# Optimization experiments

Measured on AMD Instinct MI355X. Metric: run time of the kernel, lower is better.

Reference implementation:

```python
import jax, jax.numpy as jnp
import numpy as np

NEG = -1e30

def setup_inputs() -> dict:
    key = jax.random.key(0)
    k = jax.random.split(key, 6)
    B, Lc, Lq, D = 16, 2048, 256, 256
    c = jax.random.normal(k[0], (B, Lc, D), dtype=jnp.float32)
    q = jax.random.normal(k[1], (B, Lq, D), dtype=jnp.float32)
    c_mask = jnp.ones((B, Lc), dtype=jnp.float32)
    q_mask = jnp.ones((B, Lq), dtype=jnp.float32)
    # xavier-uniform-ish scale for the similarity weights
    lim = float(np.sqrt(6.0 / (D + 1)))
    cq_weight = jax.random.uniform(k[2], (1, 1, D), jnp.float32, -lim, lim)
    c_weight = jax.random.uniform(k[3], (1, D), jnp.float32, -lim, lim)
    q_weight = jax.random.uniform(k[4], (1, D), jnp.float32, -lim, lim)
    bias = jnp.zeros((1,), dtype=jnp.float32)
    return {"c": c, "q": q, "c_mask": c_mask, "q_mask": q_mask,
            "cq_weight": cq_weight, "c_weight": c_weight,
            "q_weight": q_weight, "bias": bias}

def _masked_softmax(logits, mask):
    # mask: 1=keep, 0=pad; broadcast over logits' leading dims
    x = logits * mask + (1.0 - mask) * NEG
    return jax.nn.softmax(x, axis=-1)

def reference(c, q, c_mask, q_mask, cq_weight, c_weight, q_weight, bias):
    # trilinear similarity S[b,i,j] = w_c.c_i + w_q.q_j + (c_i*w_cq).q_j + b
    s0 = jnp.einsum('bid,od->bio', c, c_weight)              # [B,Lc,1]
    s1 = jnp.einsum('bjd,od->boj', q, q_weight)              # [B,1,Lq]
    s2 = jnp.einsum('bid,bjd->bij', c * cq_weight, q)        # [B,Lc,Lq]
    S = s0 + s1 + s2 + bias                                  # [B,Lc,Lq]
    S1 = _masked_softmax(S, q_mask[:, None, :])              # softmax over q
    C2Q = jnp.einsum('bij,bjd->bid', S1, q)                  # [B,Lc,D]
    S2t = _masked_softmax(jnp.swapaxes(S, 1, 2), c_mask[:, None, :])  # [B,Lq,Lc]
    S2 = jnp.einsum('bij,bjk->bik', S1, S2t)                 # [B,Lc,Lc]
    Q2C = jnp.einsum('bik,bkd->bid', S2, c)                  # [B,Lc,D]
    return jnp.concatenate((c, C2Q, c * C2Q, c * Q2C), axis=-1)
```

## Files before the change

kernel.cpp:

```cpp
#include <hip/hip_runtime.h>
#include <hip/hip_bf16.h>

#define NB 16
#define LC 2048
#define LQ 256
#define DD 256
#define NEGINF -1e30f

typedef __attribute__((ext_vector_type(8))) short bf16x8;
typedef __attribute__((ext_vector_type(4))) float f32x4;

#define MFMA16(a, b, c) __builtin_amdgcn_mfma_f32_16x16x32_bf16((a), (b), (c), 0, 0, 0)

typedef const unsigned int __attribute__((address_space(1))) glb_u32;
typedef unsigned int __attribute__((address_space(3))) lds_u32;

__device__ __forceinline__ void gload_lds16(const void* g, void* l) {
    __builtin_amdgcn_global_load_lds((glb_u32*)g, (lds_u32*)l, 16, 0, 0);
}

__device__ __forceinline__ short f2b(float x) {
    unsigned u = __float_as_uint(x);
    unsigned r = (u + 0x7fffu + ((u >> 16) & 1u)) >> 16;
    return (short)r;
}
__device__ __forceinline__ float b2f(short s) {
    return __uint_as_float(((unsigned)(unsigned short)s) << 16);
}

#define NCB (NB * LC / 8)
__global__ __launch_bounds__(256) void prep(
        const float* __restrict__ c, const float* __restrict__ q,
        const float* __restrict__ c_w, const float* __restrict__ cqw,
        const float* __restrict__ q_w, const float* __restrict__ bias,
        short* __restrict__ c16, float* __restrict__ s0c,
        short* __restrict__ qw16, short* __restrict__ qT16,
        float* __restrict__ s1q) {
    __shared__ float T[64][65];
    int t = threadIdx.x;
    if (blockIdx.x < NCB) {
        int row = blockIdx.x * 8 + (t >> 5);
        int k = t & 31;
        const float* src = c + (size_t)row * DD + k * 8;
        float4 v0 = *(const float4*)(src);
        float4 v1 = *(const float4*)(src + 4);
        float4 w0 = *(const float4*)(c_w + k * 8);
        float4 w1 = *(const float4*)(c_w + k * 8 + 4);
        float s = v0.x * w0.x + v0.y * w0.y + v0.z * w0.z + v0.w * w0.w
                + v1.x * w1.x + v1.y * w1.y + v1.z * w1.z + v1.w * w1.w;
        #pragma unroll
        for (int o = 16; o > 0; o >>= 1) s += __shfl_xor(s, o, 64);
        if (k == 0) s0c[row] = s;
        ushort4 o0, o1;
        o0.x = (unsigned short)f2b(v0.x); o0.y = (unsigned short)f2b(v0.y);
        o0.z = (unsigned short)f2b(v0.z); o0.w = (unsigned short)f2b(v0.w);
        o1.x = (unsigned short)f2b(v1.x); o1.y = (unsigned short)f2b(v1.y);
        o1.z = (unsigned short)f2b(v1.z); o1.w = (unsigned short)f2b(v1.w);
        ushort4* dst = (ushort4*)(c16 + (size_t)row * DD + k * 8);
        dst[0] = o0;
        dst[1] = o1;
    } else {
        int idx = blockIdx.x - NCB;
        int b = idx >> 2, j0 = (idx & 3) * 64;
        int dd = t & 63, rg = t >> 6;
        float acc[16];
        #pragma unroll
        for (int i = 0; i < 16; ++i) acc[i] = 0.f;
        for (int dc = 0; dc < 4; ++dc) {
            float wv = cqw[dc * 64 + dd];
            float qwv = q_w[dc * 64 + dd];
            #pragma unroll
            for (int rr = 0; rr < 16; ++rr) {
                int r = rg + 4 * rr;
                float v = q[((size_t)b * LQ + j0 + r) * DD + dc * 64 + dd];
                qw16[((size_t)b * LQ + j0 + r) * DD + dc * 64 + dd] = f2b(v * wv);
                acc[rr] += v * qwv;
                T[dd][r] = v;
            }
            __syncthreads();
            int jj = t & 63;
            for (int dw = t >> 6; dw < 64; dw += 4)
                qT16[((size_t)b * DD + dc * 64 + dw) * LQ + j0 + jj] = f2b(T[dw][jj]);
            __syncthreads();
        }
        float bv = bias[0];
        #pragma unroll
        for (int rr = 0; rr < 16; ++rr) {
            float s = acc[rr];
            #pragma unroll
            for (int o = 32; o > 0; o >>= 1) s += __shfl_xor(s, o, 64);
            if (dd == 0) s1q[b * LQ + j0 + rg + 4 * rr] = s + bv;
        }
    }
}

__global__ __launch_bounds__(512) void k1_S(
        const short* __restrict__ c16, const short* __restrict__ qw16,
        const float* __restrict__ cmask, const float* __restrict__ qmask,
        const float* __restrict__ s0c, const float* __restrict__ s1q,
        short* __restrict__ P1b, float* __restrict__ wgtg,
        float* __restrict__ pm, float* __restrict__ ps) {
    __shared__ short As[128 * 64];
    __shared__ short Bs[256 * 64];
    __shared__ float rmLds[128 * 4];
    __shared__ float rsLds[128 * 4];
    __shared__ float rowCLds[128];
    int b  = blockIdx.y;
    int i0 = blockIdx.x * 128;
    int t = threadIdx.x;
    int l = t & 63, w = t >> 6;
    int wr = w >> 2, wc = w & 3;

    f32x4 acc[4][4];
    #pragma unroll
    for (int m = 0; m < 4; ++m)
        #pragma unroll
        for (int n = 0; n < 4; ++n) acc[m][n] = (f32x4){0.f, 0.f, 0.f, 0.f};

    const short* Ag = c16  + ((size_t)b * LC + i0) * DD;
    const short* Bg = qw16 + ((size_t)b * LQ) * DD;
    int lrow = l >> 3;
    int lcolsw = ((l & 7) ^ lrow) * 8;

    for (int kt = 0; kt < DD; kt += 64) {
        __syncthreads();
        #pragma unroll
        for (int r = 0; r < 2; ++r) {
            int chunk = r * 8 + w;
            int row = chunk * 8 + lrow;
            gload_lds16(Ag + (size_t)row * DD + kt + lcolsw, As + chunk * 512);
        }
        #pragma unroll
        for (int r = 0; r < 4; ++r) {
            int chunk = r * 8 + w;
            int row = chunk * 8 + lrow;
            gload_lds16(Bg + (size_t)row * DD + kt + lcolsw, Bs + chunk * 512);
        }
        __syncthreads();
        #pragma unroll
        for (int kf = 0; kf < 2; ++kf) {
            bf16x8 a[4], bb[4];
            #pragma unroll
            for (int m = 0; m < 4; ++m) {
                int row = wr * 64 + m * 16 + (l & 15);
                int byte = row * 128 + kf * 64 + (l >> 4) * 16;
                a[m] = *(const bf16x8*)((const char*)As + (byte ^ ((row & 7) << 4)));
            }
            #pragma unroll
            for (int n = 0; n < 4; ++n) {
                int row = wc * 64 + n * 16 + (l & 15);
                int byte = row * 128 + kf * 64 + (l >> 4) * 16;
                bb[n] = *(const bf16x8*)((const char*)Bs + (byte ^ ((row & 7) << 4)));
            }
            #pragma unroll
            for (int m = 0; m < 4; ++m)
                #pragma unroll
                for (int n = 0; n < 4; ++n)
                    acc[m][n] = MFMA16(a[m], bb[n], acc[m][n]);
        }
    }

    float s1v[4], qmv[4], negq[4];
    #pragma unroll
    for (int n = 0; n < 4; ++n) {
        int j = wc * 64 + n * 16 + (l & 15);
        s1v[n] = s1q[b * LQ + j];
        qmv[n] = qmask[b * LQ + j];
        negq[n] = (1.f - qmv[n]) * NEGINF;
    }
    float s0r[4][4], cmr[4][4];
    #pragma unroll
    for (int m = 0; m < 4; ++m)
        #pragma unroll
        for (int reg = 0; reg < 4; ++reg) {
            int il = wr * 64 + m * 16 + (l >> 4) * 4 + reg;
            s0r[m][reg] = s0c[b * LC + i0 + il];
            cmr[m][reg] = cmask[b * LC + i0 + il];
        }
    #pragma unroll
    for (int m = 0; m < 4; ++m)
        #pragma unroll
        for (int n = 0; n < 4; ++n)
            #pragma unroll
            for (int reg = 0; reg < 4; ++reg)
                acc[m][n][reg] = acc[m][n][reg] + s0r[m][reg] + s1v[n];

    #pragma unroll
    for (int n = 0; n < 4; ++n) {
        float x2v[16];
        float mx = NEGINF;
        #pragma unroll
        for (int m = 0; m < 4; ++m)
            #pragma unroll
            for (int reg = 0; reg < 4; ++reg) {
                float cm = cmr[m][reg];
                float x2 = acc[m][n][reg] * cm + (1.f - cm) * NEGINF;
                x2v[m * 4 + reg] = x2;
                mx = fmaxf(mx, x2);
            }
        float ss = 0.f;
        #pragma unroll
        for (int e = 0; e < 16; ++e) ss += __expf(x2v[e] - mx);
        #pragma unroll
        for (int off = 16; off <= 32; off <<= 1) {
            float om = __shfl_xor(mx, off, 64);
            float os = __shfl_xor(ss, off, 64);
            float nm = fmaxf(mx, om);
            ss = ss * __expf(mx - nm) + os * __expf(om - nm);
            mx = nm;
        }
        if (l < 16) {
            size_t idx = ((size_t)b * 32 + blockIdx.x * 2 + wr) * LQ + wc * 64 + n * 16 + l;
            pm[idx] = mx;
            ps[idx] = ss;
        }
    }

    #pragma unroll
    for (int m = 0; m < 4; ++m)
        #pragma unroll
        for (int reg = 0; reg < 4; ++reg) {
            float mx = NEGINF;
            #pragma unroll
            for (int n = 0; n < 4; ++n)
                mx = fmaxf(mx, fmaf(acc[m][n][reg], qmv[n], negq[n]));
            #pragma unroll
            for (int o = 1; o <= 8; o <<= 1) mx = fmaxf(mx, __shfl_xor(mx, o, 64));
            float ss = 0.f;
            #pragma unroll
            for (int n = 0; n < 4; ++n)
                ss += __expf(fmaf(acc[m][n][reg], qmv[n], negq[n]) - mx);
            #pragma unroll
            for (int o = 1; o <= 8; o <<= 1) ss += __shfl_xor(ss, o, 64);
            if ((l & 15) == 0) {
                int row = wr * 64 + m * 16 + (l >> 4) * 4 + reg;
                rmLds[row * 4 + wc] = mx;
                rsLds[row * 4 + wc] = ss;
            }
        }
    __syncthreads();
    if (t < 128) {
        float m0 = rmLds[t * 4 + 0], m1 = rmLds[t * 4 + 1];
        float m2 = rmLds[t * 4 + 2], m3 = rmLds[t * 4 + 3];
        float mm = fmaxf(fmaxf(m0, m1), fmaxf(m2, m3));
        float ss = rsLds[t * 4 + 0] * __expf(m0 - mm)
                 + rsLds[t * 4 + 1] * __expf(m1 - mm)
                 + rsLds[t * 4 + 2] * __expf(m2 - mm)
                 + rsLds[t * 4 + 3] * __expf(m3 - mm);
        float rc = mm + logf(ss);
        rowCLds[t] = rc;
        wgtg[(size_t)b * LC + i0 + t] = cmask[b * LC + i0 + t] * __expf(rc);
    }
    __syncthreads();

    float rCv[4][4];
    #pragma unroll
    for (int m = 0; m < 4; ++m)
        #pragma unroll
        for (int reg = 0; reg < 4; ++reg)
            rCv[m][reg] = rowCLds[wr * 64 + m * 16 + (l >> 4) * 4 + reg];
    #pragma unroll
    for (int m = 0; m < 4; ++m)
        #pragma unroll
        for (int n = 0; n < 4; ++n)
            #pragma unroll
            for (int reg = 0; reg < 4; ++reg) {
                float p = __expf(fmaf(acc[m][n][reg], qmv[n], negq[n]) - rCv[m][reg]);
                int il = wr * 64 + m * 16 + (l >> 4) * 4 + reg;
                int j = wc * 64 + n * 16 + (l & 15);
                P1b[((size_t)b * LC + i0 + il) * LQ + j] = f2b(p);
            }
}

#define K3S 72
__global__ __launch_bounds__(256) void k3_A2C(
        const short* __restrict__ c16, const short* __restrict__ P1b,
        const float* __restrict__ wgtg,
        float* __restrict__ p3) {
    __shared__ short As[128 * K3S];
    __shared__ short Bs[128 * K3S];
    int b  = blockIdx.z;
    int ks = blockIdx.y;
    int d0 = (blockIdx.x >> 1) * 128;
    int j0 = (blockIdx.x & 1) * 128;
    int t = threadIdx.x, l = t & 63, w = t >> 6;
    int wr = w >> 1, wc = w & 1;

    f32x4 acc[4][4];
    #pragma unroll
    for (int m = 0; m < 4; ++m)
        #pragma unroll
        for (int n = 0; n < 4; ++n) acc[m][n] = (f32x4){0.f, 0.f, 0.f, 0.f};

    int ii4 = (t >> 4) * 4;
    int c8  = (t & 15) * 8;
    int ip  = ii4 ^ (((c8 >> 3) & 7) << 3);

    for (int k0 = ks * 512; k0 < ks * 512 + 512; k0 += 64) {
        __syncthreads();
        bf16x8 av[4], pv[4];
        float wv[4];
        #pragma unroll
        for (int r = 0; r < 4; ++r) {
            size_t gi = (size_t)b * LC + k0 + ii4 + r;
            av[r] = *(const bf16x8*)(c16 + gi * DD + d0 + c8);
            pv[r] = *(const bf16x8*)(P1b + gi * LQ + j0 + c8);
            wv[r] = wgtg[gi];
        }
        #pragma unroll
        for (int g = 0; g < 8; ++g) {
            short4 a4, b4;
            a4.x = av[0][g]; a4.y = av[1][g]; a4.z = av[2][g]; a4.w = av[3][g];
            b4.x = f2b(b2f(pv[0][g]) * wv[0]);
            b4.y = f2b(b2f(pv[1][g]) * wv[1]);
            b4.z = f2b(b2f(pv[2][g]) * wv[2]);
            b4.w = f2b(b2f(pv[3][g]) * wv[3]);
            *(short4*)(&As[(c8 + g) * K3S + ip]) = a4;
            *(short4*)(&Bs[(c8 + g) * K3S + ip]) = b4;
        }
        __syncthreads();
        #pragma unroll
        for (int kf = 0; kf < 2; ++kf) {
            bf16x8 a[4], bb[4];
            int colL = kf * 32 + (l >> 4) * 8;
            #pragma unroll
            for (int m = 0; m < 4; ++m) {
                int row = wr * 64 + m * 16 + (l & 15);
                int colP = colL ^ (((row >> 3) & 7) << 3);
                a[m] = *(const bf16x8*)((const char*)As +
                        row * (K3S * 2) + colP * 2);
            }
            #pragma unroll
            for (int n = 0; n < 4; ++n) {
                int row = wc * 64 + n * 16 + (l & 15);
                int colP = colL ^ (((row >> 3) & 7) << 3);
                bb[n] = *(const bf16x8*)((const char*)Bs +
                        row * (K3S * 2) + colP * 2);
            }
            #pragma unroll
            for (int m = 0; m < 4; ++m)
                #pragma unroll
                for (int n = 0; n < 4; ++n)
                    acc[m][n] = MFMA16(a[m], bb[n], acc[m][n]);
        }
    }
    float* P = p3 + (((size_t)b * 4 + ks) * 4 + blockIdx.x) * 16384;
    #pragma unroll
    for (int m = 0; m < 4; ++m)
        #pragma unroll
        for (int n = 0; n < 4; ++n)
            #pragma unroll
            for (int reg = 0; reg < 4; ++reg) {
                int ld = wr * 64 + m * 16 + (l >> 4) * 4 + reg;
                int lj = wc * 64 + n * 16 + (l & 15);
                P[ld * 128 + lj] = acc[m][n][reg];
            }
}

__global__ __launch_bounds__(256) void k3r_reduce(
        const float* __restrict__ p3,
        const float* __restrict__ pm, const float* __restrict__ ps,
        short* __restrict__ A2CT) {
    __shared__ float colCs[256];
    int b = blockIdx.y;
    int t = threadIdx.x;
    {
        float m = NEGINF, s = 0.f;
        for (int ch = 0; ch < 32; ++ch) {
            float pmv = pm[((size_t)b * 32 + ch) * LQ + t];
            float psv = ps[((size_t)b * 32 + ch) * LQ + t];
            float mn = fmaxf(m, pmv);
            s = s * __expf(m - mn) + psv * __expf(pmv - mn);
            m = mn;
        }
        colCs[t] = m + logf(s);
    }
    __syncthreads();
    int linear = blockIdx.x * 256 + t;
    int d = linear >> 6;
    int j4 = (linear & 63) * 4;
    int tile = (d >> 7) * 2 + (j4 >> 7);
    int ld = d & 127, lj = j4 & 127;
    const float* base = p3 + (((size_t)b * 4) * 4 + tile) * 16384 + ld * 128 + lj;
    float4 s = {0.f, 0.f, 0.f, 0.f};
    #pragma unroll
    for (int ks = 0; ks < 4; ++ks) {
        float4 v = *(const float4*)(base + (size_t)ks * 4 * 16384);
        s.x += v.x; s.y += v.y; s.z += v.z; s.w += v.w;
    }
    s.x *= __expf(-colCs[j4 + 0]);
    s.y *= __expf(-colCs[j4 + 1]);
    s.z *= __expf(-colCs[j4 + 2]);
    s.w *= __expf(-colCs[j4 + 3]);
    short4 o;
    o.x = f2b(s.x); o.y = f2b(s.y); o.z = f2b(s.z); o.w = f2b(s.w);
    *(short4*)(A2CT + ((size_t)b * DD + d) * LQ + j4) = o;
}

__global__ __launch_bounds__(256) void k4_out(
        const short* __restrict__ P1b, const short* __restrict__ qT16,
        const short* __restrict__ A2CT, const float* __restrict__ c,
        float* __restrict__ out) {
    __shared__ float Lo1[16][260];
    __shared__ float Lo2[16][260];
    int b = blockIdx.y, i0 = blockIdx.x * 64;
    int t = threadIdx.x, l = t & 63, w = t >> 6;
    int d0w = w * 64;

    f32x4 acc1[4][4], acc2[4][4];
    #pragma unroll
    for (int m = 0; m < 4; ++m)
        #pragma unroll
        for (int n = 0; n < 4; ++n) {
            acc1[m][n] = (f32x4){0.f, 0.f, 0.f, 0.f};
            acc2[m][n] = (f32x4){0.f, 0.f, 0.f, 0.f};
        }
    const short* Sr  = P1b  + ((size_t)b * LC + i0) * LQ;
    const short* qTb = qT16 + (size_t)b * DD * LQ;
    const short* aTb = A2CT + (size_t)b * DD * LQ;

    #pragma unroll 2
    for (int kf = 0; kf < 8; ++kf) {
        int j8 = kf * 32 + (l >> 4) * 8;
        bf16x8 a[4];
        #pragma unroll
        for (int m = 0; m < 4; ++m)
            a[m] = *(const bf16x8*)(Sr + (size_t)(m * 16 + (l & 15)) * LQ + j8);
        #pragma unroll
        for (int n = 0; n < 4; ++n) {
            int d = d0w + n * 16 + (l & 15);
            size_t off = (size_t)d * LQ + j8;
            bf16x8 bq = *(const bf16x8*)(qTb + off);
            bf16x8 ba = *(const bf16x8*)(aTb + off);
            #pragma unroll
            for (int m = 0; m < 4; ++m) {
                acc1[m][n] = MFMA16(a[m], bq, acc1[m][n]);
                acc2[m][n] = MFMA16(a[m], ba, acc2[m][n]);
            }
        }
    }

    const float* cb = c + (size_t)b * LC * DD;
    #pragma unroll
    for (int m = 0; m < 4; ++m) {
        __syncthreads();
        #pragma unroll
        for (int n = 0; n < 4; ++n) {
            int col = d0w + n * 16 + (l & 15);
            #pragma unroll
            for (int reg = 0; reg < 4; ++reg) {
                int row = (l >> 4) * 4 + reg;
                Lo1[row][col] = acc1[m][n][reg];
                Lo2[row][col] = acc2[m][n][reg];
            }
        }
        __syncthreads();
        #pragma unroll
        for (int rr = 0; rr < 4; ++rr) {
            int row = w * 4 + rr;
            int i = i0 + m * 16 + row;
            float4 f1 = *(const float4*)&Lo1[row][l * 4];
            float4 f2 = *(const float4*)&Lo2[row][l * 4];
            float4 cv = *(const float4*)(cb + (size_t)i * DD + l * 4);
            size_t ob = ((size_t)b * LC + i) * (size_t)(4 * DD);
            float4 p1 = {cv.x * f1.x, cv.y * f1.y, cv.z * f1.z, cv.w * f1.w};
            float4 p2 = {cv.x * f2.x, cv.y * f2.y, cv.z * f2.z, cv.w * f2.w};
            *(float4*)(out + ob + l * 4)       = cv;
            *(float4*)(out + ob + 256 + l * 4) = f1;
            *(float4*)(out + ob + 512 + l * 4) = p1;
            *(float4*)(out + ob + 768 + l * 4) = p2;
        }
    }
}

extern "C" void kernel_launch(void* const* d_in, const int* in_sizes, int n_in,
                              void* d_out, int out_size, void* d_ws, size_t ws_size,
                              hipStream_t stream) {
    const float* c     = (const float*)d_in[0];
    const float* q     = (const float*)d_in[1];
    const float* cmask = (const float*)d_in[2];
    const float* qmask = (const float*)d_in[3];
    const float* cqw   = (const float*)d_in[4];
    const float* c_w   = (const float*)d_in[5];
    const float* q_w   = (const float*)d_in[6];
    const float* bias  = (const float*)d_in[7];
    float* out = (float*)d_out;

    char* w = (char*)d_ws;
    short* P1b   = (short*)(w);
    short* c16   = (short*)(w + 16777216);
    short* qw16  = (short*)(w + 33554432);
    short* qT16  = (short*)(w + 35651584);
    short* A2CT  = (short*)(w + 37748736);
    float* s0c   = (float*)(w + 39845888);
    float* s1q   = (float*)(w + 39976960);
    float* pm    = (float*)(w + 39993344);
    float* ps    = (float*)(w + 40517632);
    float* wgtg  = (float*)(w + 41041920);
    float* p3    = (float*)(w + 41172992);

    prep<<<dim3(NCB + NB * LQ / 64), dim3(256), 0, stream>>>(
        c, q, c_w, cqw, q_w, bias, c16, s0c, qw16, qT16, s1q);
    k1_S<<<dim3(LC / 128, NB), dim3(512), 0, stream>>>(
        c16, qw16, cmask, qmask, s0c, s1q, P1b, wgtg, pm, ps);
    k3_A2C<<<dim3(4, 4, NB), dim3(256), 0, stream>>>(
        c16, P1b, wgtg, p3);
    k3r_reduce<<<dim3(64, NB), dim3(256), 0, stream>>>(p3, pm, ps, A2CT);
    k4_out<<<dim3(LC / 64, NB), dim3(256), 0, stream>>>(
        P1b, qT16, A2CT, c, out);
}
```

Before: 119.9 us.

## Fuse split-K reduce into A2C GEMM and move c passthrough into prep

The A2C GEMM drops its 4-way split-K and absorbs the separate reduce kernel, so the column log-sum-exp and normalization happen in its epilogue. This removes the fp32 partial-sum buffer round trip and one kernel launch. In exchange the grid shrinks to 64 blocks, each running the full 2048-long K loop; a register double-buffer prefetch is added to hide load latency. The fp32 copy of c into the output is now written in prep, and the output kernel reads bf16 c16 instead of fp32 c for its products. That cuts read bandwidth but lowers the precision of c*C2Q and c*Q2C.

```diff
diff --git a/kernel.cpp b/kernel.cpp
--- a/kernel.cpp
+++ b/kernel.cpp
@@ -35,7 +35,7 @@
         const float* __restrict__ q_w, const float* __restrict__ bias,
         short* __restrict__ c16, float* __restrict__ s0c,
         short* __restrict__ qw16, short* __restrict__ qT16,
-        float* __restrict__ s1q) {
+        float* __restrict__ s1q, float* __restrict__ out) {
     __shared__ float T[64][65];
     int t = threadIdx.x;
     if (blockIdx.x < NCB) {
@@ -51,6 +51,9 @@
         #pragma unroll
         for (int o = 16; o > 0; o >>= 1) s += __shfl_xor(s, o, 64);
         if (k == 0) s0c[row] = s;
+        size_t ob = (size_t)row * (size_t)(4 * DD) + k * 8;
+        *(float4*)(out + ob)     = v0;
+        *(float4*)(out + ob + 4) = v1;
         ushort4 o0, o1;
         o0.x = (unsigned short)f2b(v0.x); o0.y = (unsigned short)f2b(v0.y);
         o0.z = (unsigned short)f2b(v0.z); o0.w = (unsigned short)f2b(v0.w);
@@ -276,16 +279,29 @@
 __global__ __launch_bounds__(256) void k3_A2C(
         const short* __restrict__ c16, const short* __restrict__ P1b,
         const float* __restrict__ wgtg,
-        float* __restrict__ p3) {
+        const float* __restrict__ pm, const float* __restrict__ ps,
+        short* __restrict__ A2CT) {
     __shared__ short As[128 * K3S];
     __shared__ short Bs[128 * K3S];
-    int b  = blockIdx.z;
-    int ks = blockIdx.y;
+    __shared__ float colCs[128];
+    int b  = blockIdx.y;
     int d0 = (blockIdx.x >> 1) * 128;
     int j0 = (blockIdx.x & 1) * 128;
     int t = threadIdx.x, l = t & 63, w = t >> 6;
     int wr = w >> 1, wc = w & 1;
 
+    if (t < 128) {
+        float m = NEGINF, s = 0.f;
+        for (int ch = 0; ch < 32; ++ch) {
+            float pmv = pm[((size_t)b * 32 + ch) * LQ + j0 + t];
+            float psv = ps[((size_t)b * 32 + ch) * LQ + j0 + t];
+            float mn = fmaxf(m, pmv);
+            s = s * __expf(m - mn) + psv * __expf(pmv - mn);
+            m = mn;
+        }
+        colCs[t] = m + logf(s);
+    }
+
     f32x4 acc[4][4];
     #pragma unroll
     for (int m = 0; m < 4; ++m)
@@ -295,28 +311,38 @@
     int ii4 = (t >> 4) * 4;
     int c8  = (t & 15) * 8;
     int ip  = ii4 ^ (((c8 >> 3) & 7) << 3);
-
-    for (int k0 = ks * 512; k0 < ks * 512 + 512; k0 += 64) {
-        __syncthreads();
-        bf16x8 av[4], pv[4];
-        float wv[4];
-        #pragma unroll
-        for (int r = 0; r < 4; ++r) {
-            size_t gi = (size_t)b * LC + k0 + ii4 + r;
-            av[r] = *(const bf16x8*)(c16 + gi * DD + d0 + c8);
-            pv[r] = *(const bf16x8*)(P1b + gi * LQ + j0 + c8);
-            wv[r] = wgtg[gi];
-        }
+    const size_t gbase = (size_t)b * LC;
+
+    bf16x8 avA[4], pvA[4]; float wvA[4];
+    bf16x8 avB[4], pvB[4]; float wvB[4];
+
+    #pragma unroll
+    for (int r = 0; r < 4; ++r) {
+        size_t gi = gbase + ii4 + r;
+        avA[r] = *(const bf16x8*)(c16 + gi * DD + d0 + c8);
+        pvA[r] = *(const bf16x8*)(P1b + gi * LQ + j0 + c8);
+        wvA[r] = wgtg[gi];
+    }
+
+    for (int k0 = 0; k0 < LC; k0 += 128) {
+        __syncthreads();
         #pragma unroll
         for (int g = 0; g < 8; ++g) {
             short4 a4, b4;
-            a4.x = av[0][g]; a4.y = av[1][g]; a4.z = av[2][g]; a4.w = av[3][g];
-            b4.x = f2b(b2f(pv[0][g]) * wv[0]);
-            b4.y = f2b(b2f(pv[1][g]) * wv[1]);
-            b4.z = f2b(b2f(pv[2][g]) * wv[2]);
-            b4.w = f2b(b2f(pv[3][g]) * wv[3]);
+            a4.x = avA[0][g]; a4.y = avA[1][g]; a4.z = avA[2][g]; a4.w = avA[3][g];
+            b4.x = f2b(b2f(pvA[0][g]) * wvA[0]);
+            b4.y = f2b(b2f(pvA[1][g]) * wvA[1]);
+            b4.z = f2b(b2f(pvA[2][g]) * wvA[2]);
+            b4.w = f2b(b2f(pvA[3][g]) * wvA[3]);
             *(short4*)(&As[(c8 + g) * K3S + ip]) = a4;
             *(short4*)(&Bs[(c8 + g) * K3S + ip]) = b4;
+        }
+        #pragma unroll
+        for (int r = 0; r < 4; ++r) {
+            size_t gi = gbase + k0 + 64 + ii4 + r;
+            avB[r] = *(const bf16x8*)(c16 + gi * DD + d0 + c8);
+            pvB[r] = *(const bf16x8*)(P1b + gi * LQ + j0 + c8);
+            wvB[r] = wgtg[gi];
         }
         __syncthreads();
         #pragma unroll
@@ -327,15 +353,13 @@
             for (int m = 0; m < 4; ++m) {
                 int row = wr * 64 + m * 16 + (l & 15);
                 int colP = colL ^ (((row >> 3) & 7) << 3);
-                a[m] = *(const bf16x8*)((const char*)As +
-                        row * (K3S * 2) + colP * 2);
+                a[m] = *(const bf16x8*)((const char*)As + row * (K3S * 2) + colP * 2);
             }
             #pragma unroll
             for (int n = 0; n < 4; ++n) {
                 int row = wc * 64 + n * 16 + (l & 15);
                 int colP = colL ^ (((row >> 3) & 7) << 3);
-                bb[n] = *(const bf16x8*)((const char*)Bs +
-                        row * (K3S * 2) + colP * 2);
+                bb[n] = *(const bf16x8*)((const char*)Bs + row * (K3S * 2) + colP * 2);
             }
             #pragma unroll
             for (int m = 0; m < 4; ++m)
@@ -343,63 +367,71 @@
                 for (int n = 0; n < 4; ++n)
                     acc[m][n] = MFMA16(a[m], bb[n], acc[m][n]);
         }
-    }
-    float* P = p3 + (((size_t)b * 4 + ks) * 4 + blockIdx.x) * 16384;
+        __syncthreads();
+        #pragma unroll
+        for (int g = 0; g < 8; ++g) {
+            short4 a4, b4;
+            a4.x = avB[0][g]; a4.y = avB[1][g]; a4.z = avB[2][g]; a4.w = avB[3][g];
+            b4.x = f2b(b2f(pvB[0][g]) * wvB[0]);
+            b4.y = f2b(b2f(pvB[1][g]) * wvB[1]);
+            b4.z = f2b(b2f(pvB[2][g]) * wvB[2]);
+            b4.w = f2b(b2f(pvB[3][g]) * wvB[3]);
+            *(short4*)(&As[(c8 + g) * K3S + ip]) = a4;
+            *(short4*)(&Bs[(c8 + g) * K3S + ip]) = b4;
+        }
+        if (k0 + 128 < LC) {
+            #pragma unroll
+            for (int r = 0; r < 4; ++r) {
+                size_t gi = gbase + k0 + 128 + ii4 + r;
+                avA[r] = *(const bf16x8*)(c16 + gi * DD + d0 + c8);
+                pvA[r] = *(const bf16x8*)(P1b + gi * LQ + j0 + c8);
+                wvA[r] = wgtg[gi];
+            }
+        }
+        __syncthreads();
+        #pragma unroll
+        for (int kf = 0; kf < 2; ++kf) {
+            bf16x8 a[4], bb[4];
+            int colL = kf * 32 + (l >> 4) * 8;
+            #pragma unroll
+            for (int m = 0; m < 4; ++m) {
+                int row = wr * 64 + m * 16 + (l & 15);
+                int colP = colL ^ (((row >> 3) & 7) << 3);
+                a[m] = *(const bf16x8*)((const char*)As + row * (K3S * 2) + colP * 2);
+            }
+            #pragma unroll
+            for (int n = 0; n < 4; ++n) {
+                int row = wc * 64 + n * 16 + (l & 15);
+                int colP = colL ^ (((row >> 3) & 7) << 3);
+                bb[n] = *(const bf16x8*)((const char*)Bs + row * (K3S * 2) + colP * 2);
+            }
+            #pragma unroll
+            for (int m = 0; m < 4; ++m)
+                #pragma unroll
+                for (int n = 0; n < 4; ++n)
+                    acc[m][n] = MFMA16(a[m], bb[n], acc[m][n]);
+        }
+    }
+
+    float ec[4];
+    #pragma unroll
+    for (int n = 0; n < 4; ++n)
+        ec[n] = __expf(-colCs[wc * 64 + n * 16 + (l & 15)]);
     #pragma unroll
     for (int m = 0; m < 4; ++m)
         #pragma unroll
         for (int n = 0; n < 4; ++n)
             #pragma unroll
             for (int reg = 0; reg < 4; ++reg) {
-                int ld = wr * 64 + m * 16 + (l >> 4) * 4 + reg;
-                int lj = wc * 64 + n * 16 + (l & 15);
-                P[ld * 128 + lj] = acc[m][n][reg];
-            }
-}
-
-__global__ __launch_bounds__(256) void k3r_reduce(
-        const float* __restrict__ p3,
-        const float* __restrict__ pm, const float* __restrict__ ps,
-        short* __restrict__ A2CT) {
-    __shared__ float colCs[256];
-    int b = blockIdx.y;
-    int t = threadIdx.x;
-    {
-        float m = NEGINF, s = 0.f;
-        for (int ch = 0; ch < 32; ++ch) {
-            float pmv = pm[((size_t)b * 32 + ch) * LQ + t];
-            float psv = ps[((size_t)b * 32 + ch) * LQ + t];
-            float mn = fmaxf(m, pmv);
-            s = s * __expf(m - mn) + psv * __expf(pmv - mn);
-            m = mn;
-        }
-        colCs[t] = m + logf(s);
-    }
-    __syncthreads();
-    int linear = blockIdx.x * 256 + t;
-    int d = linear >> 6;
-    int j4 = (linear & 63) * 4;
-    int tile = (d >> 7) * 2 + (j4 >> 7);
-    int ld = d & 127, lj = j4 & 127;
-    const float* base = p3 + (((size_t)b * 4) * 4 + tile) * 16384 + ld * 128 + lj;
-    float4 s = {0.f, 0.f, 0.f, 0.f};
-    #pragma unroll
-    for (int ks = 0; ks < 4; ++ks) {
-        float4 v = *(const float4*)(base + (size_t)ks * 4 * 16384);
-        s.x += v.x; s.y += v.y; s.z += v.z; s.w += v.w;
-    }
-    s.x *= __expf(-colCs[j4 + 0]);
-    s.y *= __expf(-colCs[j4 + 1]);
-    s.z *= __expf(-colCs[j4 + 2]);
-    s.w *= __expf(-colCs[j4 + 3]);
-    short4 o;
-    o.x = f2b(s.x); o.y = f2b(s.y); o.z = f2b(s.z); o.w = f2b(s.w);
-    *(short4*)(A2CT + ((size_t)b * DD + d) * LQ + j4) = o;
+                int d = d0 + wr * 64 + m * 16 + (l >> 4) * 4 + reg;
+                int j = j0 + wc * 64 + n * 16 + (l & 15);
+                A2CT[((size_t)b * DD + d) * LQ + j] = f2b(acc[m][n][reg] * ec[n]);
+            }
 }
 
 __global__ __launch_bounds__(256) void k4_out(
         const short* __restrict__ P1b, const short* __restrict__ qT16,
-        const short* __restrict__ A2CT, const float* __restrict__ c,
+        const short* __restrict__ A2CT, const short* __restrict__ c16,
         float* __restrict__ out) {
     __shared__ float Lo1[16][260];
     __shared__ float Lo2[16][260];
@@ -440,7 +472,7 @@
         }
     }
 
-    const float* cb = c + (size_t)b * LC * DD;
+    const short* cb16 = c16 + (size_t)b * LC * DD;
     #pragma unroll
     for (int m = 0; m < 4; ++m) {
         __syncthreads();
@@ -461,11 +493,11 @@
             int i = i0 + m * 16 + row;
             float4 f1 = *(const float4*)&Lo1[row][l * 4];
             float4 f2 = *(const float4*)&Lo2[row][l * 4];
-            float4 cv = *(const float4*)(cb + (size_t)i * DD + l * 4);
+            short4 cu = *(const short4*)(cb16 + (size_t)i * DD + l * 4);
+            float c0 = b2f(cu.x), c1 = b2f(cu.y), c2 = b2f(cu.z), c3 = b2f(cu.w);
             size_t ob = ((size_t)b * LC + i) * (size_t)(4 * DD);
-            float4 p1 = {cv.x * f1.x, cv.y * f1.y, cv.z * f1.z, cv.w * f1.w};
-            float4 p2 = {cv.x * f2.x, cv.y * f2.y, cv.z * f2.z, cv.w * f2.w};
-            *(float4*)(out + ob + l * 4)       = cv;
+            float4 p1 = {c0 * f1.x, c1 * f1.y, c2 * f1.z, c3 * f1.w};
+            float4 p2 = {c0 * f2.x, c1 * f2.y, c2 * f2.z, c3 * f2.w};
             *(float4*)(out + ob + 256 + l * 4) = f1;
             *(float4*)(out + ob + 512 + l * 4) = p1;
             *(float4*)(out + ob + 768 + l * 4) = p2;
@@ -497,15 +529,13 @@
     float* pm    = (float*)(w + 39993344);
     float* ps    = (float*)(w + 40517632);
     float* wgtg  = (float*)(w + 41041920);
-    float* p3    = (float*)(w + 41172992);
 
     prep<<<dim3(NCB + NB * LQ / 64), dim3(256), 0, stream>>>(
-        c, q, c_w, cqw, q_w, bias, c16, s0c, qw16, qT16, s1q);
+        c, q, c_w, cqw, q_w, bias, c16, s0c, qw16, qT16, s1q, out);
     k1_S<<<dim3(LC / 128, NB), dim3(512), 0, stream>>>(
         c16, qw16, cmask, qmask, s0c, s1q, P1b, wgtg, pm, ps);
-    k3_A2C<<<dim3(4, 4, NB), dim3(256), 0, stream>>>(
-        c16, P1b, wgtg, p3);
-    k3r_reduce<<<dim3(64, NB), dim3(256), 0, stream>>>(p3, pm, ps, A2CT);
+    k3_A2C<<<dim3(4, NB), dim3(256), 0, stream>>>(
+        c16, P1b, wgtg, pm, ps, A2CT);
     k4_out<<<dim3(LC / 64, NB), dim3(256), 0, stream>>>(
-        P1b, qT16, A2CT, c, out);
-}
+        P1b, qT16, A2CT, c16, out);
+}
```

After: 129.8 us. 1.08x slower.
